# Optimization experiments

Measured on AMD Instinct MI355X. Metric: run time of the kernel, lower is better.

The kernel has to match this reference:

```python
import jax, jax.numpy as jnp
import numpy as np

ALPHA = 1.0


def setup_inputs() -> dict:
    key = jax.random.key(0)
    k1, k2 = jax.random.split(key)
    B, K, D = 65536, 256, 768
    embeddings = jax.random.normal(k1, (B, D), dtype=jnp.float32)
    centroids = jax.random.normal(k2, (K, D), dtype=jnp.float32)
    return {"embeddings": embeddings, "centroids": centroids}


def reference(embeddings, centroids):
    # Batched L2 cdist via the (|e|^2 + |c|^2 - 2 e.c) expansion; avoids the
    # per-sample Python loop in the original and never materializes [B,K,D].
    e2 = jnp.sum(embeddings * embeddings, axis=-1, keepdims=True)      # [B,1]
    c2 = jnp.sum(centroids * centroids, axis=-1)                       # [K]
    d2 = e2 + c2[None, :] - 2.0 * (embeddings @ centroids.T)          # [B,K]
    dist = jnp.sqrt(jnp.maximum(d2, 0.0))                              # [B,K]

    predicted_labels = jnp.argmin(dist, axis=1)                        # [B]

    # Faithful to source: transpose to [K,B]; softmin is over the BATCH axis
    # per centroid, and the final mean is over centroids.
    dT = dist.T                                                        # [K,B]
    minv = jnp.min(dT, axis=1, keepdims=True)                          # [K,1]
    exps = jnp.exp(-ALPHA * (dT - minv))                               # [K,B]
    softmin = exps / jnp.sum(exps, axis=1, keepdims=True)              # [K,B]
    clustering_loss = jnp.mean(jnp.sum(dT * softmin, axis=1))          # scalar

    return clustering_loss, predicted_labels
```

## Files before the change

kernel.cpp:

```cpp
#include <hip/hip_runtime.h>
#include <math.h>
#include <float.h>

#define D_DIM 768
#define K_C   256
#define KC    32
#define NCH   24
#define BMR   128
#define NTHR  512
#define MAXFIX 32768
#define MARGIN 6e-3f
#define M0SHIFT 39.0f

typedef __attribute__((ext_vector_type(8))) short s16x8;
typedef __attribute__((ext_vector_type(4))) float f32x4;

__device__ inline unsigned short f2bf(float x) {
    unsigned u = __float_as_uint(x);
    unsigned r = 0x7FFFu + ((u >> 16) & 1u);
    return (unsigned short)((u + r) >> 16);
}
__device__ inline int swz(int row, int slot) {
    return row*32 + (((slot ^ (row >> 1)) & 3) << 3);
}
__device__ inline void gl_lds16(const void* g, void* l) {
    __builtin_amdgcn_global_load_lds(
        (const __attribute__((address_space(1))) void*)g,
        (__attribute__((address_space(3))) void*)l, 16, 0, 0);
}
__device__ inline unsigned pk2(float a, float b) {
    return __builtin_amdgcn_perm(__float_as_uint(b), __float_as_uint(a), 0x07060302u);
}
__device__ inline float hi_of(float x) {
    return __uint_as_float(__float_as_uint(x) & 0xFFFF0000u);
}

__global__ __launch_bounds__(256) void kprep(const float* __restrict__ C,
    short* __restrict__ Cimg, float* __restrict__ c2f, int* __restrict__ fix_cnt,
    float* __restrict__ out)
{
    const int k = blockIdx.x;
    const int t = threadIdx.x;
    __shared__ double red[4];
    double s = 0.0;
#pragma unroll
    for (int i = 0; i < 3; ++i) {
        int d = t + 256*i;
        float x = C[(size_t)k*D_DIM + d];
        s += (double)x * (double)x;
        int ch = d >> 5, g = (d & 31) >> 3, e = d & 7;
        Cimg[(size_t)ch*8192 + swz(k, g) + e] = (short)f2bf(x);
    }
#pragma unroll
    for (int m = 1; m < 64; m <<= 1) s += __shfl_xor(s, m, 64);
    if ((t & 63) == 0) red[t >> 6] = s;
    __syncthreads();
    if (t == 0) {
        c2f[k] = (float)(red[0] + red[1] + red[2] + red[3]);
        if (k == 0) { *fix_cnt = 0; out[0] = 0.f; }
    }
}

#define ECONV_M(Q0,Q1,EHI) do {                                         \
        e2p = fmaf(Q0.x,Q0.x,e2p); e2p = fmaf(Q0.y,Q0.y,e2p);           \
        e2p = fmaf(Q0.z,Q0.z,e2p); e2p = fmaf(Q0.w,Q0.w,e2p);           \
        e2p = fmaf(Q1.x,Q1.x,e2p); e2p = fmaf(Q1.y,Q1.y,e2p);           \
        e2p = fmaf(Q1.z,Q1.z,e2p); e2p = fmaf(Q1.w,Q1.w,e2p);           \
        uint4 Ha, La;                                                   \
        Ha.x = pk2(Q0.x,Q0.y); Ha.y = pk2(Q0.z,Q0.w);                   \
        Ha.z = pk2(Q1.x,Q1.y); Ha.w = pk2(Q1.z,Q1.w);                   \
        La.x = pk2(Q0.x-hi_of(Q0.x), Q0.y-hi_of(Q0.y));                 \
        La.y = pk2(Q0.z-hi_of(Q0.z), Q0.w-hi_of(Q0.w));                 \
        La.z = pk2(Q1.x-hi_of(Q1.x), Q1.y-hi_of(Q1.y));                 \
        La.w = pk2(Q1.z-hi_of(Q1.z), Q1.w-hi_of(Q1.w));                 \
        *reinterpret_cast<uint4*>((EHI) + ebyte) = Ha;                  \
        *reinterpret_cast<uint4*>((EHI) + 8192 + ebyte) = La;           \
    } while (0)

#define MFMA_M(EB,CB) do {                                              \
        s16x8 ah_[4], al_[4];                                           \
        _Pragma("unroll")                                               \
        for (int m_ = 0; m_ < 4; ++m_) {                                \
            ah_[m_] = *reinterpret_cast<const s16x8*>((EB) + aoff[m_]); \
            al_[m_] = *reinterpret_cast<const s16x8*>((EB) + 8192 + aoff[m_]); \
        }                                                               \
        _Pragma("unroll")                                               \
        for (int n_ = 0; n_ < 4; ++n_) {                                \
            s16x8 bh_ = *reinterpret_cast<const s16x8*>((CB) + boff[n_]); \
            _Pragma("unroll")                                           \
            for (int m_ = 0; m_ < 4; ++m_)                              \
                acc[m_][n_] = __builtin_amdgcn_mfma_f32_16x16x32_bf16(ah_[m_], bh_, acc[m_][n_], 0, 0, 0); \
            _Pragma("unroll")                                           \
            for (int m_ = 0; m_ < 4; ++m_)                              \
                acc[m_][n_] = __builtin_amdgcn_mfma_f32_16x16x32_bf16(al_[m_], bh_, acc[m_][n_], 0, 0, 0); \
        }                                                               \
    } while (0)

#define CSTAGE_M(CHI,DST) do {                                          \
        const char* img_ = (const char*)Cimg + (size_t)(CHI)*16384;     \
        gl_lds16(img_ + t*16,        (DST) + t*16);                     \
        gl_lds16(img_ + 8192 + t*16, (DST) + 8192 + t*16);              \
    } while (0)

#define WAITBAR(N) do {                                                 \
        asm volatile("s_waitcnt vmcnt(" #N ") lgkmcnt(0)" ::: "memory");\
        __builtin_amdgcn_s_barrier();                                   \
        __builtin_amdgcn_sched_barrier(0);                              \
    } while (0)

#define EQLOAD(QV0,QV1,CHI) do {                                        \
        const float* ep_ = Ep + (CHI)*KC;                               \
        QV0 = *reinterpret_cast<const float4*>(ep_);                    \
        QV1 = *reinterpret_cast<const float4*>(ep_ + 4);                \
    } while (0)

__global__ __launch_bounds__(NTHR, 4) void kdist(const float* __restrict__ E,
    const short* __restrict__ Cimg, const float* __restrict__ c2f,
    float* __restrict__ labels, float* __restrict__ partials,
    int* __restrict__ fix_cnt, int* __restrict__ fix_list)
{
    __shared__ __align__(16) char lds[65536];
    float*  e2s   = (float*)lds;
    float*  spart = (float*)(lds + 512);
    float4* topb  = (float4*)(lds + 4608);

    const int t    = threadIdx.x;
    const int lane = t & 63;
    const int w    = t >> 6;
    const int wm   = w >> 2, wn = w & 3;
    const int c4   = lane & 15, sgr = lane >> 4;
    const int R0   = blockIdx.x * BMR;

    f32x4 acc[4][4];
#pragma unroll
    for (int m = 0; m < 4; ++m)
#pragma unroll
        for (int n = 0; n < 4; ++n) acc[m][n] = (f32x4){0.f,0.f,0.f,0.f};

    const int erow = t >> 2, eseg = t & 3;
    const float* Ep = E + (size_t)(R0 + erow)*D_DIM + eseg*8;
    const int ebyte = 2*swz(erow, eseg);
    int aoff[4], boff[4];
#pragma unroll
    for (int m = 0; m < 4; ++m) aoff[m] = 2*swz(wm*64 + m*16 + c4, sgr);
#pragma unroll
    for (int n = 0; n < 4; ++n) boff[n] = 2*swz(wn*64 + n*16 + c4, sgr);
    float e2p = 0.f;
    float4 qa0, qa1, qb0, qb1;

    CSTAGE_M(0, lds + 32768);
    EQLOAD(qa0, qa1, 0);
    ECONV_M(qa0, qa1, lds);
    EQLOAD(qb0, qb1, 1);
    asm volatile("s_waitcnt lgkmcnt(0)" ::: "memory");
    __builtin_amdgcn_s_barrier();
    __builtin_amdgcn_sched_barrier(0);

#pragma unroll 1
    for (int pr = 0; pr < 11; ++pr) {
        const int ch = 2*pr;
        CSTAGE_M(ch + 1, lds + 49152);
        __builtin_amdgcn_sched_barrier(0);
        EQLOAD(qa0, qa1, ch + 2);
        MFMA_M(lds, lds + 32768);
        ECONV_M(qb0, qb1, lds + 16384);
        WAITBAR(2);
        CSTAGE_M(ch + 2, lds + 32768);
        __builtin_amdgcn_sched_barrier(0);
        EQLOAD(qb0, qb1, ch + 3);
        MFMA_M(lds + 16384, lds + 49152);
        ECONV_M(qa0, qa1, lds);
        WAITBAR(2);
    }
    CSTAGE_M(23, lds + 49152);
    MFMA_M(lds, lds + 32768);
    ECONV_M(qb0, qb1, lds + 16384);
    WAITBAR(0);
    MFMA_M(lds + 16384, lds + 49152);
    __syncthreads();

    {
        float es = e2p + __shfl_xor(e2p, 1, 64);
        es += __shfl_xor(es, 2, 64);
        if ((t & 3) == 0) e2s[t >> 2] = es;
    }
    __syncthreads();

    float e2r[4][4];
#pragma unroll
    for (int m = 0; m < 4; ++m)
#pragma unroll
        for (int g = 0; g < 4; ++g)
            e2r[m][g] = e2s[wm*64 + m*16 + sgr*4 + g];
    float c2v[4];
#pragma unroll
    for (int n = 0; n < 4; ++n) c2v[n] = c2f[wn*64 + n*16 + c4];

#pragma unroll
    for (int m = 0; m < 4; ++m)
#pragma unroll
        for (int n = 0; n < 4; ++n) {
            f32x4 v = acc[m][n];
#pragma unroll
            for (int g = 0; g < 4; ++g) {
                float d2 = fmaf(-2.f, v[g], e2r[m][g] + c2v[n]);
                v[g] = sqrtf(fmaxf(d2, 0.f));
            }
            acc[m][n] = v;
        }

#pragma unroll
    for (int m = 0; m < 4; ++m)
#pragma unroll
        for (int g = 0; g < 4; ++g) {
            float k1 = FLT_MAX, k2 = FLT_MAX, k3 = FLT_MAX;
#pragma unroll
            for (int n = 0; n < 4; ++n) {
                unsigned idx = (unsigned)(wn*64 + n*16 + c4);
                unsigned u = __float_as_uint(acc[m][n][g]);
                float kd = __uint_as_float(((u - idx + 127u) & 0xFFFFFF00u) | idx);
                if (kd < k1)      { k3 = k2; k2 = k1; k1 = kd; }
                else if (kd < k2) { k3 = k2; k2 = kd; }
                else if (kd < k3) { k3 = kd; }
            }
#pragma unroll
            for (int msk = 1; msk < 16; msk <<= 1) {
                float o1 = __shfl_xor(k1, msk, 64);
                float o2 = __shfl_xor(k2, msk, 64);
                float o3 = __shfl_xor(k3, msk, 64);
                float m1 = fminf(k1, o1), M1 = fmaxf(k1, o1);
                float m2 = fminf(k2, o2), M2 = fmaxf(k2, o2);
                float r3 = fminf(k3, o3);
                k1 = m1;
                k2 = fminf(M1, m2);
                k3 = fminf(fmaxf(M1, m2), fminf(M2, r3));
            }
            if (c4 == 0)
                topb[wn*BMR + wm*64 + m*16 + sgr*4 + g] = (float4){k1, k2, k3, 0.f};
        }

#pragma unroll
    for (int n = 0; n < 4; ++n) {
        float s1 = 0.f, s2 = 0.f;
#pragma unroll
        for (int m = 0; m < 4; ++m)
#pragma unroll
            for (int g = 0; g < 4; ++g) {
                float d = acc[m][n][g];
                float wgt = __expf(M0SHIFT - d);
                s1 += wgt; s2 = fmaf(d, wgt, s2);
            }
        s1 += __shfl_xor(s1, 16, 64); s2 += __shfl_xor(s2, 16, 64);
        s1 += __shfl_xor(s1, 32, 64); s2 += __shfl_xor(s2, 32, 64);
        if (lane < 16) {
            int cc = wn*64 + n*16 + c4;
            float* p = &spart[(size_t)(wm*K_C + cc)*2];
            p[0] = s1; p[1] = s2;
        }
    }
    __syncthreads();

    if (t < BMR) {
        float4 q0 = topb[t],           q1 = topb[BMR + t];
        float4 q2 = topb[2*BMR + t],   q3 = topb[3*BMR + t];
#define MRG3(A1,A2,A3,B1,B2,B3,R1,R2,R3) do {                           \
        float m1_ = fminf(A1,B1), M1_ = fmaxf(A1,B1);                   \
        float m2_ = fminf(A2,B2), M2_ = fmaxf(A2,B2);                   \
        float r3_ = fminf(A3,B3);                                       \
        R1 = m1_; R2 = fminf(M1_, m2_);                                 \
        R3 = fminf(fmaxf(M1_, m2_), fminf(M2_, r3_)); } while (0)
        float a1, a2, a3, b1, b2, b3, k1, k2, k3;
        MRG3(q0.x,q0.y,q0.z, q1.x,q1.y,q1.z, a1,a2,a3);
        MRG3(q2.x,q2.y,q2.z, q3.x,q3.y,q3.z, b1,b2,b3);
        MRG3(a1,a2,a3, b1,b2,b3, k1,k2,k3);
#undef MRG3
        unsigned u1 = __float_as_uint(k1), u2 = __float_as_uint(k2), u3 = __float_as_uint(k3);
        int i1 = (int)(u1 & 255u), i2 = (int)(u2 & 255u), i3 = (int)(u3 & 255u);
        float v1 = __uint_as_float(u1 & 0xFFFFFF00u);
        float v2 = __uint_as_float(u2 & 0xFFFFFF00u);
        int row = R0 + t;
        labels[row] = (float)i1;
        if (v2 - v1 < MARGIN) {
            int slot = atomicAdd(fix_cnt, 1);
            if (slot < MAXFIX) {
                fix_list[slot*4+0] = row;
                fix_list[slot*4+1] = i1;
                fix_list[slot*4+2] = i2;
                fix_list[slot*4+3] = i3;
            }
        }
    }
    if (t < K_C) {
        float s1 = spart[(size_t)t*2]     + spart[(size_t)(K_C + t)*2];
        float s2 = spart[(size_t)t*2 + 1] + spart[(size_t)(K_C + t)*2 + 1];
        partials[((size_t)blockIdx.x*K_C + t)*2]     = s1;
        partials[((size_t)blockIdx.x*K_C + t)*2 + 1] = s2;
    }
}

__global__ __launch_bounds__(256) void krefB(const float* __restrict__ E,
    const float* __restrict__ C, const int* __restrict__ fix_cnt,
    const int* __restrict__ fix_list, float* __restrict__ labels)
{
    int cnt = *fix_cnt; if (cnt > MAXFIX) cnt = MAXFIX;
    int lane = threadIdx.x & 63;
    int wv = (int)((blockIdx.x * blockDim.x + threadIdx.x) >> 6);
    const int NW = (gridDim.x * blockDim.x) >> 6;
    for (int e = wv; e < cnt; e += NW) {
        int row = fix_list[e*4+0];
        int k1  = fix_list[e*4+1], k2 = fix_list[e*4+2], k3 = fix_list[e*4+3];
        double s1 = 0, s2 = 0, s3 = 0;
        for (int d = lane; d < D_DIM; d += 64) {
            double ed = (double)E[(size_t)row*D_DIM + d];
            double ca = (double)C[(size_t)k1*D_DIM + d];
            double cb = (double)C[(size_t)k2*D_DIM + d];
            double cc = (double)C[(size_t)k3*D_DIM + d];
            s1 += ca*(ca - 2.0*ed);
            s2 += cb*(cb - 2.0*ed);
            s3 += cc*(cc - 2.0*ed);
        }
#pragma unroll
        for (int msk = 32; msk; msk >>= 1) {
            s1 += __shfl_down(s1, msk, 64);
            s2 += __shfl_down(s2, msk, 64);
            s3 += __shfl_down(s3, msk, 64);
        }
        if (lane == 0) {
            double bv = s1; int bk = k1;
            if (s2 < bv || (s2 == bv && k2 < bk)) { bv = s2; bk = k2; }
            if (s3 < bv || (s3 == bv && k3 < bk)) { bv = s3; bk = k3; }
            labels[row] = (float)bk;
        }
    }
}

__global__ __launch_bounds__(256) void kcol(const float* __restrict__ partials,
                                            float* __restrict__ out, int NB)
{
    __shared__ float W1[4], W2[4];
    const int c = blockIdx.x;
    const int t = threadIdx.x;
    float s1 = 0.f, s2 = 0.f;
    for (int b = t; b < NB; b += 256) {
        const float* p = &partials[((size_t)b*K_C + c)*2];
        s1 += p[0]; s2 += p[1];
    }
#pragma unroll
    for (int msk = 1; msk < 64; msk <<= 1) {
        s1 += __shfl_xor(s1, msk, 64);
        s2 += __shfl_xor(s2, msk, 64);
    }
    int lane = t & 63, wv = t >> 6;
    if (lane == 0) { W1[wv] = s1; W2[wv] = s2; }
    __syncthreads();
    if (t == 0) {
        float a = W1[0] + W1[1] + W1[2] + W1[3];
        float b = W2[0] + W2[1] + W2[2] + W2[3];
        atomicAdd(out, (b / a) * (1.0f / 256.0f));
    }
}

extern "C" void kernel_launch(void* const* d_in, const int* in_sizes, int n_in,
                              void* d_out, int out_size, void* d_ws, size_t ws_size,
                              hipStream_t stream)
{
    const float* E = (const float*)d_in[0];
    const float* C = (const float*)d_in[1];
    float* out = (float*)d_out;

    const int Bn = in_sizes[0] / D_DIM;
    const int NB = Bn / BMR;

    char* ws = (char*)d_ws;
    float* c2f      = (float*)ws;
    int*   fix_cnt  = (int*)(ws + 1024);
    int*   fix_list = (int*)(ws + 1088);
    short* Cimg     = (short*)(ws + 1088 + MAXFIX*16);
    float* partials = (float*)((char*)Cimg + (size_t)NCH*16384);
    float* labels   = out + 1;

    kprep <<<K_C, 256, 0, stream>>>(C, Cimg, c2f, fix_cnt, out);
    kdist <<<NB,  NTHR, 0, stream>>>(E, Cimg, c2f, labels, partials,
                                     fix_cnt, fix_list);
    krefB <<<128, 256, 0, stream>>>(E, C, fix_cnt, fix_list, labels);
    kcol  <<<K_C, 256, 0, stream>>>(partials, out, NB);
}
```

Baseline: 95.07 us.

## Fuse near-tie label refinement and column reduction into distance kernel

Moves the fp64 refinement of ambiguous argmin rows into the tail of the main distance kernel, using a per-block LDS queue instead of a global fix list, which removes the separate refinement launch. Per-block column partials are now accumulated with global float atomics into 256-entry arrays, and a single-block finalize replaces the per-column reduction kernel. This cuts two kernel launches and the partials round trip through memory. In exchange it adds atomic contention on 512 addresses and a serial tail per block when many rows are near ties, and the float atomic summation order becomes nondeterministic.

```diff
diff --git a/kernel.cpp b/kernel.cpp
--- a/kernel.cpp
+++ b/kernel.cpp
@@ -8,7 +8,6 @@
 #define NCH   24
 #define BMR   128
 #define NTHR  512
-#define MAXFIX 32768
 #define MARGIN 6e-3f
 #define M0SHIFT 39.0f
 
@@ -36,8 +35,8 @@
 }
 
 __global__ __launch_bounds__(256) void kprep(const float* __restrict__ C,
-    short* __restrict__ Cimg, float* __restrict__ c2f, int* __restrict__ fix_cnt,
-    float* __restrict__ out)
+    short* __restrict__ Cimg, float* __restrict__ c2f,
+    float* __restrict__ g1, float* __restrict__ g2)
 {
     const int k = blockIdx.x;
     const int t = threadIdx.x;
@@ -57,7 +56,7 @@
     __syncthreads();
     if (t == 0) {
         c2f[k] = (float)(red[0] + red[1] + red[2] + red[3]);
-        if (k == 0) { *fix_cnt = 0; out[0] = 0.f; }
+        g1[k] = 0.f; g2[k] = 0.f;
     }
 }
 
@@ -115,14 +114,16 @@
     } while (0)
 
 __global__ __launch_bounds__(NTHR, 4) void kdist(const float* __restrict__ E,
-    const short* __restrict__ Cimg, const float* __restrict__ c2f,
-    float* __restrict__ labels, float* __restrict__ partials,
-    int* __restrict__ fix_cnt, int* __restrict__ fix_list)
+    const float* __restrict__ Cf, const short* __restrict__ Cimg,
+    const float* __restrict__ c2f, float* __restrict__ labels,
+    float* __restrict__ g1, float* __restrict__ g2)
 {
     __shared__ __align__(16) char lds[65536];
     float*  e2s   = (float*)lds;
     float*  spart = (float*)(lds + 512);
     float4* topb  = (float4*)(lds + 4608);
+    int*    qcnt  = (int*)(lds + 12800);
+    int4*   qlist = (int4*)(lds + 12816);
 
     const int t    = threadIdx.x;
     const int lane = t & 63;
@@ -183,6 +184,7 @@
         float es = e2p + __shfl_xor(e2p, 1, 64);
         es += __shfl_xor(es, 2, 64);
         if ((t & 3) == 0) e2s[t >> 2] = es;
+        if (t == 0) *qcnt = 0;
     }
     __syncthreads();
 
@@ -281,40 +283,29 @@
         int row = R0 + t;
         labels[row] = (float)i1;
         if (v2 - v1 < MARGIN) {
-            int slot = atomicAdd(fix_cnt, 1);
-            if (slot < MAXFIX) {
-                fix_list[slot*4+0] = row;
-                fix_list[slot*4+1] = i1;
-                fix_list[slot*4+2] = i2;
-                fix_list[slot*4+3] = i3;
-            }
+            int slot = atomicAdd(qcnt, 1);
+            qlist[slot] = make_int4(row, i1, i2, i3);
         }
     }
     if (t < K_C) {
         float s1 = spart[(size_t)t*2]     + spart[(size_t)(K_C + t)*2];
         float s2 = spart[(size_t)t*2 + 1] + spart[(size_t)(K_C + t)*2 + 1];
-        partials[((size_t)blockIdx.x*K_C + t)*2]     = s1;
-        partials[((size_t)blockIdx.x*K_C + t)*2 + 1] = s2;
-    }
-}
-
-__global__ __launch_bounds__(256) void krefB(const float* __restrict__ E,
-    const float* __restrict__ C, const int* __restrict__ fix_cnt,
-    const int* __restrict__ fix_list, float* __restrict__ labels)
-{
-    int cnt = *fix_cnt; if (cnt > MAXFIX) cnt = MAXFIX;
-    int lane = threadIdx.x & 63;
-    int wv = (int)((blockIdx.x * blockDim.x + threadIdx.x) >> 6);
-    const int NW = (gridDim.x * blockDim.x) >> 6;
-    for (int e = wv; e < cnt; e += NW) {
-        int row = fix_list[e*4+0];
-        int k1  = fix_list[e*4+1], k2 = fix_list[e*4+2], k3 = fix_list[e*4+3];
+        atomicAdd(&g1[t], s1);
+        atomicAdd(&g2[t], s2);
+    }
+    __syncthreads();
+
+    const int nq = *qcnt;
+    for (int e = w; e < nq; e += 8) {
+        int4 q = qlist[e];
+        const int row = q.x, k1 = q.y, k2 = q.z, k3 = q.w;
         double s1 = 0, s2 = 0, s3 = 0;
+#pragma unroll 1
         for (int d = lane; d < D_DIM; d += 64) {
             double ed = (double)E[(size_t)row*D_DIM + d];
-            double ca = (double)C[(size_t)k1*D_DIM + d];
-            double cb = (double)C[(size_t)k2*D_DIM + d];
-            double cc = (double)C[(size_t)k3*D_DIM + d];
+            double ca = (double)Cf[(size_t)k1*D_DIM + d];
+            double cb = (double)Cf[(size_t)k2*D_DIM + d];
+            double cc = (double)Cf[(size_t)k3*D_DIM + d];
             s1 += ca*(ca - 2.0*ed);
             s2 += cb*(cb - 2.0*ed);
             s3 += cc*(cc - 2.0*ed);
@@ -334,30 +325,17 @@
     }
 }
 
-__global__ __launch_bounds__(256) void kcol(const float* __restrict__ partials,
-                                            float* __restrict__ out, int NB)
+__global__ __launch_bounds__(256) void kfin(const float* __restrict__ g1,
+    const float* __restrict__ g2, float* __restrict__ out)
 {
-    __shared__ float W1[4], W2[4];
-    const int c = blockIdx.x;
-    const int t = threadIdx.x;
-    float s1 = 0.f, s2 = 0.f;
-    for (int b = t; b < NB; b += 256) {
-        const float* p = &partials[((size_t)b*K_C + c)*2];
-        s1 += p[0]; s2 += p[1];
-    }
-#pragma unroll
-    for (int msk = 1; msk < 64; msk <<= 1) {
-        s1 += __shfl_xor(s1, msk, 64);
-        s2 += __shfl_xor(s2, msk, 64);
-    }
-    int lane = t & 63, wv = t >> 6;
-    if (lane == 0) { W1[wv] = s1; W2[wv] = s2; }
-    __syncthreads();
-    if (t == 0) {
-        float a = W1[0] + W1[1] + W1[2] + W1[3];
-        float b = W2[0] + W2[1] + W2[2] + W2[3];
-        atomicAdd(out, (b / a) * (1.0f / 256.0f));
-    }
+    __shared__ float Ws[4];
+    int t = threadIdx.x;
+    float v = g2[t] / g1[t];
+#pragma unroll
+    for (int msk = 1; msk < 64; msk <<= 1) v += __shfl_xor(v, msk, 64);
+    if ((t & 63) == 0) Ws[t >> 6] = v;
+    __syncthreads();
+    if (t == 0) out[0] = (Ws[0] + Ws[1] + Ws[2] + Ws[3]) / 256.0f;
 }
 
 extern "C" void kernel_launch(void* const* d_in, const int* in_sizes, int n_in,
@@ -372,16 +350,13 @@
     const int NB = Bn / BMR;
 
     char* ws = (char*)d_ws;
-    float* c2f      = (float*)ws;
-    int*   fix_cnt  = (int*)(ws + 1024);
-    int*   fix_list = (int*)(ws + 1088);
-    short* Cimg     = (short*)(ws + 1088 + MAXFIX*16);
-    float* partials = (float*)((char*)Cimg + (size_t)NCH*16384);
-    float* labels   = out + 1;
-
-    kprep <<<K_C, 256, 0, stream>>>(C, Cimg, c2f, fix_cnt, out);
-    kdist <<<NB,  NTHR, 0, stream>>>(E, Cimg, c2f, labels, partials,
-                                     fix_cnt, fix_list);
-    krefB <<<128, 256, 0, stream>>>(E, C, fix_cnt, fix_list, labels);
-    kcol  <<<K_C, 256, 0, stream>>>(partials, out, NB);
-}
+    float* c2f  = (float*)ws;
+    float* g1   = (float*)(ws + 1024);
+    float* g2   = (float*)(ws + 2048);
+    short* Cimg = (short*)(ws + 4096);
+    float* labels = out + 1;
+
+    kprep <<<K_C, 256, 0, stream>>>(C, Cimg, c2f, g1, g2);
+    kdist <<<NB,  NTHR, 0, stream>>>(E, C, Cimg, c2f, labels, g1, g2);
+    kfin  <<<1,   256, 0, stream>>>(g1, g2, out);
+}
```

New measurement: 81.78 us. -14.0%, faster.
